# Optimization experiments

Measured on AMD Instinct MI355X. Metric: run time of the kernel, lower is better.

The kernel has to match this reference:

```python
import jax, jax.numpy as jnp
import numpy as np

N = 131072   # total nodes in batch
D = 128      # hidden dim (in_dim = out_dim = 128)
DX = 64      # raw node feature dim (x and rw_feature each)
NG = 1024    # number of graphs (global_add_pool segments)
E = 4194304  # edges per hop adjacency (avg degree 32)
H = 4        # num_hops + 1 MLP branches per layer


def setup_inputs() -> dict:
    key = jax.random.key(0)
    ks = jax.random.split(key, 16)
    s = 0.05
    return {
        "x": jax.random.normal(ks[0], (N, DX), jnp.float32),
        "rw_feature": jax.random.normal(ks[1], (N, DX), jnp.float32),
        "hop1_features": jax.random.normal(ks[2], (N, D), jnp.float32),
        "hop2_features": jax.random.normal(ks[3], (N, D), jnp.float32),
        "hop3_features": jax.random.normal(ks[4], (N, D), jnp.float32),
        "hop1_edges": jax.random.randint(ks[5], (2, E), 0, N, dtype=jnp.int32),
        "hop2_edges": jax.random.randint(ks[6], (2, E), 0, N, dtype=jnp.int32),
        "hop3_edges": jax.random.randint(ks[7], (2, E), 0, N, dtype=jnp.int32),
        "batch": jnp.sort(jax.random.randint(ks[8], (N,), 0, NG, dtype=jnp.int32)),
        "l1_w1": jax.random.normal(ks[9], (H, D, D), jnp.float32) * s,
        "l1_b1": jnp.zeros((H, D), jnp.float32),
        "l1_w2": jax.random.normal(ks[10], (H, D, D), jnp.float32) * s,
        "l1_b2": jnp.zeros((H, D), jnp.float32),
        "l2_w1": jax.random.normal(ks[11], (H, D, D), jnp.float32) * s,
        "l2_b1": jnp.zeros((H, D), jnp.float32),
        "l2_w2": jax.random.normal(ks[12], (H, D, D), jnp.float32) * s,
        "l2_b2": jnp.zeros((H, D), jnp.float32),
        "lin_w": jax.random.normal(ks[13], (2 * D, D), jnp.float32) * s,
        "lin_b": jnp.zeros((D,), jnp.float32),
    }


def _mhc_layer(hops, w1, b1, w2, b2):
    # hops: [H, N, D]; per-hop MLP (Linear -> ReLU -> Dropout(eval) -> Linear), summed over hops
    z = jax.nn.relu(jnp.einsum('hni,hio->hno', hops, w1) + b1[:, None, :])
    y = jnp.einsum('hno,hop->hnp', z, w2) + b2[:, None, :]
    return jnp.sum(y, axis=0)  # [N, D]


def _spmm(edges, x):
    # torch.sparse.mm(A, x) with A[r, c] = 1.0 per edge; duplicate edges accumulate (COO sum)
    return jax.ops.segment_sum(x[edges[1]], edges[0], num_segments=N)


def reference(x, rw_feature, hop1_features, hop2_features, hop3_features,
              hop1_edges, hop2_edges, hop3_edges, batch,
              l1_w1, l1_b1, l1_w2, l1_b2, l2_w1, l2_b1, l2_w2, l2_b2,
              lin_w, lin_b):
    f = jnp.concatenate([x, rw_feature], axis=1)  # [N, D]
    h1 = jnp.stack([f, hop1_features, hop2_features, hop3_features], axis=0)  # [H, N, D]
    x1 = _mhc_layer(h1, l1_w1, l1_b1, l1_w2, l1_b2)
    h2 = jnp.stack([x1,
                    _spmm(hop1_edges, x1),
                    _spmm(hop2_edges, x1),
                    _spmm(hop3_edges, x1)], axis=0)
    x2 = _mhc_layer(h2, l2_w1, l2_b1, l2_w2, l2_b2)
    out = jnp.concatenate([x1, x2], axis=1) @ lin_w + lin_b  # concat=True path
    return jax.ops.segment_sum(out, batch, num_segments=NG)  # global_add_pool -> [NG, D]
```

## Files before the change

kernel.cpp:

```cpp
#include <hip/hip_runtime.h>

#define N_NODES 131072
#define DIM     128
#define NGRAPH  1024
#define NEDGE   4194304

#define NW      512
#define WBINS   256
#define NSL     256
#define SLICE_E (NEDGE / NSL)
#define CAP     12288

typedef float floatx4 __attribute__((ext_vector_type(4)));
typedef float f32x4  __attribute__((ext_vector_type(4)));
typedef __bf16 bf16x8 __attribute__((ext_vector_type(8)));
typedef __bf16 bf16x4 __attribute__((ext_vector_type(4)));

__device__ __forceinline__ int lds_off(int row, int kb) {
    return row * 256 + (kb ^ ((row & 7) << 4));
}

__global__ __launch_bounds__(256)
void zero_kernel(floatx4* __restrict__ p, long n4) {
    long i = (long)blockIdx.x * blockDim.x + threadIdx.x;
    long stride = (long)gridDim.x * blockDim.x;
    floatx4 z = {0.f, 0.f, 0.f, 0.f};
    for (; i < n4; i += stride) p[i] = z;
}

__global__ __launch_bounds__(256)
void tr_kernel(const float* __restrict__ src, __bf16* __restrict__ dst, int nmat) {
    int idx = blockIdx.x * blockDim.x + threadIdx.x;
    int total = nmat * 16384;
    if (idx >= total) return;
    int m = idx >> 14;
    int col = (idx >> 7) & 127;
    int k = idx & 127;
    dst[idx] = (__bf16)src[m * 16384 + k * 128 + col];
}

__global__ __launch_bounds__(256)
void wincount_kernel(const int* __restrict__ e1, const int* __restrict__ e2,
                     const int* __restrict__ e3, int* __restrict__ gcount) {
    const int gb = blockIdx.x;
    const int sl = gb % NSL;
    const int hop = gb / NSL;
    const int* rows = hop == 0 ? e1 : hop == 1 ? e2 : e3;

    __shared__ int cnt[NW];
    for (int i = threadIdx.x; i < NW; i += 256) cnt[i] = 0;
    __syncthreads();

    const int4* src = (const int4*)rows + (size_t)sl * (SLICE_E / 4);
    for (int j = threadIdx.x; j < SLICE_E / 4; j += 256) {
        int4 v = src[j];
        atomicAdd(&cnt[v.x >> 8], 1); atomicAdd(&cnt[v.y >> 8], 1);
        atomicAdd(&cnt[v.z >> 8], 1); atomicAdd(&cnt[v.w >> 8], 1);
    }
    __syncthreads();

    int* dst = gcount + ((size_t)hop * NSL + sl) * NW;
    for (int i = threadIdx.x; i < NW; i += 256) dst[i] = cnt[i];
}

__global__ __launch_bounds__(256)
void basescan_kernel(const int* __restrict__ gcount, int* __restrict__ baseo,
                     int* __restrict__ wbase) {
    const int hop = blockIdx.x;
    const int t = threadIdx.x;
    __shared__ int wt[NW];
    __shared__ int part[256];

    for (int k = 0; k < 2; ++k) {
        int w = t * 2 + k;
        int s = 0;
        for (int sl = 0; sl < NSL; ++sl)
            s += gcount[((size_t)hop * NSL + sl) * NW + w];
        wt[w] = s;
    }
    __syncthreads();
    part[t] = wt[2 * t] + wt[2 * t + 1];
    __syncthreads();
    for (int d = 1; d < 256; d <<= 1) {
        int v = (t >= d) ? part[t - d] : 0;
        __syncthreads();
        part[t] += v;
        __syncthreads();
    }
    int run = (t == 0) ? 0 : part[t - 1];
    for (int k = 0; k < 2; ++k) {
        int w = 2 * t + k;
        wbase[hop * (NW + 1) + w] = run;
        int r2 = run;
        for (int sl = 0; sl < NSL; ++sl) {
            baseo[((size_t)hop * NW + w) * NSL + sl] = r2;
            r2 += gcount[((size_t)hop * NSL + sl) * NW + w];
        }
        run += wt[w];
    }
    if (t == 255) wbase[hop * (NW + 1) + NW] = NEDGE;
}

__global__ __launch_bounds__(256)
void bucket_kernel(const int* __restrict__ e1, const int* __restrict__ e2,
                   const int* __restrict__ e3, const int* __restrict__ baseo,
                   int* __restrict__ buf) {
    const int gb = blockIdx.x;
    const int sl = gb % NSL;
    const int hop = gb / NSL;
    const int* rows = hop == 0 ? e1 : hop == 1 ? e2 : e3;
    const int* cs = rows + NEDGE;

    __shared__ int cur[NW];
    for (int i = threadIdx.x; i < NW; i += 256)
        cur[i] = baseo[((size_t)hop * NW + i) * NSL + sl];
    __syncthreads();

    int* b = buf + (size_t)hop * NEDGE;
    const int4* r4 = (const int4*)rows + (size_t)sl * (SLICE_E / 4);
    const int4* c4 = (const int4*)cs + (size_t)sl * (SLICE_E / 4);
    for (int j = threadIdx.x; j < SLICE_E / 4; j += 256) {
        int4 r = r4[j];
        int4 c = c4[j];
        int p;
        p = atomicAdd(&cur[r.x >> 8], 1); b[p] = ((r.x & 255) << 17) | c.x;
        p = atomicAdd(&cur[r.y >> 8], 1); b[p] = ((r.y & 255) << 17) | c.y;
        p = atomicAdd(&cur[r.z >> 8], 1); b[p] = ((r.z & 255) << 17) | c.z;
        p = atomicAdd(&cur[r.w >> 8], 1); b[p] = ((r.w & 255) << 17) | c.w;
    }
}

__global__ __launch_bounds__(256)
void winbuild_kernel(const int* __restrict__ buf, const int* __restrict__ wbase,
                     int* __restrict__ offs3, int* __restrict__ cols) {
    const int gb = blockIdx.x;
    const int w = gb % NW;
    const int hop = gb / NW;
    const int b0 = wbase[hop * (NW + 1) + w];
    const int b1 = wbase[hop * (NW + 1) + w + 1];
    const int tot = b1 - b0;
    const int* src = buf + (size_t)hop * NEDGE + b0;
    int* col = cols + (size_t)hop * NEDGE;
    int* offs = offs3 + (size_t)hop * (N_NODES + 1);
    const int t = threadIdx.x;

    __shared__ int hist[WBINS];
    __shared__ int scanb[WBINS];
    __shared__ int image[CAP];

    hist[t] = 0;
    __syncthreads();
    for (int i = t; i < tot; i += 256) atomicAdd(&hist[src[i] >> 17], 1);
    __syncthreads();

    int v = hist[t];
    scanb[t] = v;
    __syncthreads();
    for (int d = 1; d < 256; d <<= 1) {
        int u = (t >= d) ? scanb[t - d] : 0;
        __syncthreads();
        scanb[t] += u;
        __syncthreads();
    }
    const int excl = scanb[t] - v;

    offs[w * WBINS + t] = b0 + excl;
    if (w == NW - 1 && t == 0) offs[N_NODES] = NEDGE;
    __syncthreads();

    if (tot <= CAP) {
        hist[t] = excl;
        __syncthreads();
        for (int i = t; i < tot; i += 256) {
            int e = src[i];
            int p = atomicAdd(&hist[e >> 17], 1);
            image[p] = e & 0x1FFFF;
        }
        __syncthreads();
        for (int i = t; i < tot; i += 256) col[b0 + i] = image[i];
    } else {
        hist[t] = b0 + excl;
        __syncthreads();
        for (int i = t; i < tot; i += 256) {
            int e = src[i];
            int p = atomicAdd(&hist[e >> 17], 1);
            col[p] = e & 0x1FFFF;
        }
    }
}

__global__ __launch_bounds__(256)
void csr_spmm_kernel(const int* __restrict__ offs, const int* __restrict__ col,
                     const __bf16* __restrict__ xin, __bf16* __restrict__ outb) {
    const int lane = threadIdx.x & 63;
    const int row = blockIdx.x * (blockDim.x >> 6) + (threadIdx.x >> 6);
    if (row >= N_NODES) return;
    const int beg = offs[row];
    const int end = offs[row + 1];

    float a0 = 0.f, a1 = 0.f, b0 = 0.f, b1 = 0.f;
    float c0f = 0.f, c1f = 0.f, d0 = 0.f, d1 = 0.f;
    for (int b = beg; b < end; b += 64) {
        const int n = min(64, end - b);
        int cidx = (b + lane < end) ? col[b + lane] : 0;
        int i = 0;
        for (; i + 4 <= n; i += 4) {
            int e0 = __shfl(cidx, i);
            int e1 = __shfl(cidx, i + 1);
            int e2 = __shfl(cidx, i + 2);
            int e3 = __shfl(cidx, i + 3);
            unsigned v0 = *(const unsigned*)(xin + (size_t)e0 * 128 + lane * 2);
            unsigned v1 = *(const unsigned*)(xin + (size_t)e1 * 128 + lane * 2);
            unsigned v2 = *(const unsigned*)(xin + (size_t)e2 * 128 + lane * 2);
            unsigned v3 = *(const unsigned*)(xin + (size_t)e3 * 128 + lane * 2);
            a0 += __uint_as_float(v0 << 16); a1 += __uint_as_float(v0 & 0xffff0000u);
            b0 += __uint_as_float(v1 << 16); b1 += __uint_as_float(v1 & 0xffff0000u);
            c0f += __uint_as_float(v2 << 16); c1f += __uint_as_float(v2 & 0xffff0000u);
            d0 += __uint_as_float(v3 << 16); d1 += __uint_as_float(v3 & 0xffff0000u);
        }
        for (; i < n; ++i) {
            int e = __shfl(cidx, i);
            unsigned v = *(const unsigned*)(xin + (size_t)e * 128 + lane * 2);
            a0 += __uint_as_float(v << 16); a1 += __uint_as_float(v & 0xffff0000u);
        }
    }
    float o0 = a0 + b0 + c0f + d0;
    float o1 = a1 + b1 + c1f + d1;
    union { unsigned u; __bf16 h[2]; } pk;
    pk.h[0] = (__bf16)o0; pk.h[1] = (__bf16)o1;
    *(unsigned*)(outb + (size_t)row * 128 + lane * 2) = pk.u;
}

__device__ __forceinline__ void stage_bf16_tile(char* dst, const __bf16* src, int tid) {
#pragma unroll
    for (int it = 0; it < 8; ++it) {
        int c = tid + it * 256;
        int r = c >> 4, o = c & 15;
        uint4 v = *(const uint4*)(src + (size_t)r * 128 + o * 8);
        *(uint4*)(dst + lds_off(r, o * 16)) = v;
    }
}

__device__ __forceinline__ void stage_f32_tile(char* dst, const float* src, int tid) {
#pragma unroll
    for (int it = 0; it < 16; ++it) {
        int c = tid + it * 256;
        int r = c >> 5, o = c & 31;
        floatx4 v = *(const floatx4*)(src + (size_t)r * 128 + o * 4);
        bf16x4 h;
        h[0] = (__bf16)v[0]; h[1] = (__bf16)v[1];
        h[2] = (__bf16)v[2]; h[3] = (__bf16)v[3];
        *(bf16x4*)(dst + lds_off(r, o * 8)) = h;
    }
}

__device__ __forceinline__ void mfma_relu_phase(char* az, const char* wb,
                                                const float* bias,
                                                int r0, int lrow, int grp) {
    bf16x8 am[2][4];
#pragma unroll
    for (int mt = 0; mt < 2; ++mt)
#pragma unroll
        for (int kk = 0; kk < 4; ++kk)
            am[mt][kk] = *(const bf16x8*)(az + lds_off(r0 + mt * 16 + lrow,
                                                       kk * 64 + grp * 16));
#pragma unroll
    for (int n = 0; n < 8; ++n) {
        f32x4 a0 = {0.f, 0.f, 0.f, 0.f};
        f32x4 a1 = {0.f, 0.f, 0.f, 0.f};
#pragma unroll
        for (int kk = 0; kk < 4; ++kk) {
            bf16x8 b = *(const bf16x8*)(wb + lds_off(n * 16 + lrow,
                                                     kk * 64 + grp * 16));
            a0 = __builtin_amdgcn_mfma_f32_16x16x32_bf16(am[0][kk], b, a0, 0, 0, 0);
            a1 = __builtin_amdgcn_mfma_f32_16x16x32_bf16(am[1][kk], b, a1, 0, 0, 0);
        }
        float bs = bias[n * 16 + lrow];
#pragma unroll
        for (int rg = 0; rg < 4; ++rg) {
            float v0 = fmaxf(a0[rg] + bs, 0.f);
            float v1 = fmaxf(a1[rg] + bs, 0.f);
            *(__bf16*)(az + lds_off(r0 + grp * 4 + rg, (n * 16 + lrow) * 2)) = (__bf16)v0;
            *(__bf16*)(az + lds_off(r0 + 16 + grp * 4 + rg, (n * 16 + lrow) * 2)) = (__bf16)v1;
        }
    }
}

__device__ __forceinline__ void mfma_phase(const char* az, const char* wb,
                                           int r0, int lrow, int grp,
                                           f32x4 (&acc)[2][8]) {
    bf16x8 am[2][4];
#pragma unroll
    for (int mt = 0; mt < 2; ++mt)
#pragma unroll
        for (int kk = 0; kk < 4; ++kk)
            am[mt][kk] = *(const bf16x8*)(az + lds_off(r0 + mt * 16 + lrow,
                                                       kk * 64 + grp * 16));
#pragma unroll
    for (int kk = 0; kk < 4; ++kk)
#pragma unroll
        for (int n = 0; n < 8; ++n) {
            bf16x8 b = *(const bf16x8*)(wb + lds_off(n * 16 + lrow,
                                                     kk * 64 + grp * 16));
#pragma unroll
            for (int mt = 0; mt < 2; ++mt)
                acc[mt][n] = __builtin_amdgcn_mfma_f32_16x16x32_bf16(
                    am[mt][kk], b, acc[mt][n], 0, 0, 0);
        }
}

__global__ __launch_bounds__(256, 2)
void layer1_kernel(const float* __restrict__ x, const float* __restrict__ rw,
                   const float* __restrict__ f1, const float* __restrict__ f2,
                   const float* __restrict__ f3,
                   const __bf16* __restrict__ wt1, const float* __restrict__ b1,
                   const __bf16* __restrict__ wt2, const float* __restrict__ b2,
                   __bf16* __restrict__ x1out)
{
    __shared__ uint4 lds_u4[4096];
    char* AZ = (char*)lds_u4;
    char* WB = (char*)lds_u4 + 32768;
    const int tid = threadIdx.x;
    const int lane = tid & 63;
    const int w = tid >> 6;
    const int r0 = w * 32;
    const int lrow = lane & 15;
    const int grp = lane >> 4;
    const int row0 = blockIdx.x * 128;

    f32x4 Y[2][8];
#pragma unroll
    for (int mt = 0; mt < 2; ++mt)
#pragma unroll
        for (int n = 0; n < 8; ++n) Y[mt][n] = {0.f, 0.f, 0.f, 0.f};

    for (int h = 0; h < 4; ++h) {
        __syncthreads();
        if (h == 0) {
#pragma unroll
            for (int it = 0; it < 16; ++it) {
                int c = tid + it * 256;
                int r = c >> 5, o = c & 31;
                const float* src = (o < 16)
                    ? (x  + (size_t)(row0 + r) * 64 + o * 4)
                    : (rw + (size_t)(row0 + r) * 64 + (o - 16) * 4);
                floatx4 v = *(const floatx4*)src;
                bf16x4 hh;
                hh[0] = (__bf16)v[0]; hh[1] = (__bf16)v[1];
                hh[2] = (__bf16)v[2]; hh[3] = (__bf16)v[3];
                *(bf16x4*)(AZ + lds_off(r, o * 8)) = hh;
            }
        } else {
            const float* feat = (h == 1) ? f1 : (h == 2) ? f2 : f3;
            stage_f32_tile(AZ, feat + (size_t)row0 * 128, tid);
        }
        stage_bf16_tile(WB, wt1 + (size_t)h * 16384, tid);
        __syncthreads();

        mfma_relu_phase(AZ, WB, b1 + h * 128, r0, lrow, grp);

        __syncthreads();
        stage_bf16_tile(WB, wt2 + (size_t)h * 16384, tid);
        __syncthreads();
        mfma_phase(AZ, WB, r0, lrow, grp, Y);
    }

#pragma unroll
    for (int n = 0; n < 8; ++n) {
        int cc = n * 16 + lrow;
        float bs = b2[cc] + b2[128 + cc] + b2[256 + cc] + b2[384 + cc];
#pragma unroll
        for (int mt = 0; mt < 2; ++mt)
#pragma unroll
            for (int rg = 0; rg < 4; ++rg) {
                int zr = r0 + mt * 16 + grp * 4 + rg;
                *(__bf16*)(AZ + lds_off(zr, cc * 2)) = (__bf16)(Y[mt][n][rg] + bs);
            }
    }
    __syncthreads();
#pragma unroll
    for (int it = 0; it < 8; ++it) {
        int f = tid + it * 256;
        int r = f >> 4, o = f & 15;
        uint4 v = *(const uint4*)(AZ + lds_off(r, o * 16));
        *(uint4*)(x1out + (size_t)(row0 + r) * 128 + o * 8) = v;
    }
}

__global__ __launch_bounds__(256, 2)
void layer2_kernel(const __bf16* __restrict__ x1b, const __bf16* __restrict__ s1,
                   const __bf16* __restrict__ s2, const __bf16* __restrict__ s3,
                   const __bf16* __restrict__ wt1, const float* __restrict__ b1,
                   const __bf16* __restrict__ wt2, const float* __restrict__ b2,
                   const __bf16* __restrict__ wtl, const float* __restrict__ linb,
                   const int* __restrict__ batch, float* __restrict__ dout)
{
    __shared__ uint4 lds_u4[4096];
    char* AZ = (char*)lds_u4;
    char* WB = (char*)lds_u4 + 32768;
    const int tid = threadIdx.x;
    const int lane = tid & 63;
    const int w = tid >> 6;
    const int r0 = w * 32;
    const int lrow = lane & 15;
    const int grp = lane >> 4;
    const int row0 = blockIdx.x * 128;

    f32x4 Y[2][8];
#pragma unroll
    for (int mt = 0; mt < 2; ++mt)
#pragma unroll
        for (int n = 0; n < 8; ++n) Y[mt][n] = {0.f, 0.f, 0.f, 0.f};

    for (int h = 0; h < 4; ++h) {
        const __bf16* feat = (h == 0) ? x1b : (h == 1) ? s1 : (h == 2) ? s2 : s3;
        __syncthreads();
        stage_bf16_tile(AZ, feat + (size_t)row0 * 128, tid);
        stage_bf16_tile(WB, wt1 + (size_t)h * 16384, tid);
        __syncthreads();

        mfma_relu_phase(AZ, WB, b1 + h * 128, r0, lrow, grp);

        __syncthreads();
        stage_bf16_tile(WB, wt2 + (size_t)h * 16384, tid);
        __syncthreads();
        mfma_phase(AZ, WB, r0, lrow, grp, Y);
    }

#pragma unroll
    for (int n = 0; n < 8; ++n) {
        int cc = n * 16 + lrow;
        float bs = b2[cc] + b2[128 + cc] + b2[256 + cc] + b2[384 + cc];
#pragma unroll
        for (int mt = 0; mt < 2; ++mt)
#pragma unroll
            for (int rg = 0; rg < 4; ++rg) {
                float v = Y[mt][n][rg] + bs;
                int zr = r0 + mt * 16 + grp * 4 + rg;
                *(__bf16*)(AZ + lds_off(zr, (n * 16 + lrow) * 2)) = (__bf16)v;
            }
    }
    __syncthreads();
    stage_bf16_tile(WB, wtl + 16384, tid);
    __syncthreads();

    f32x4 o[2][8];
#pragma unroll
    for (int mt = 0; mt < 2; ++mt)
#pragma unroll
        for (int n = 0; n < 8; ++n) o[mt][n] = {0.f, 0.f, 0.f, 0.f};
    mfma_phase(AZ, WB, r0, lrow, grp, o);

    __syncthreads();
    stage_bf16_tile(AZ, x1b + (size_t)row0 * 128, tid);
    stage_bf16_tile(WB, wtl, tid);
    __syncthreads();
    mfma_phase(AZ, WB, r0, lrow, grp, o);

    __syncthreads();
    float* tile32 = (float*)lds_u4;
#pragma unroll
    for (int n = 0; n < 8; ++n) {
        int cc = n * 16 + lrow;
        float lb = linb[cc];
#pragma unroll
        for (int mt = 0; mt < 2; ++mt)
#pragma unroll
            for (int rg = 0; rg < 4; ++rg) {
                int rl = r0 + mt * 16 + grp * 4 + rg;
                tile32[rl * 128 + cc] = o[mt][n][rg] + lb;
            }
    }
    __syncthreads();

    if (tid < 128) {
        const int d = tid;
        float acc = 0.f;
        int cur = batch[row0];
        for (int r = 0; r < 128; ++r) {
            int b = batch[row0 + r];
            if (b != cur) {
                atomicAdd(dout + (size_t)cur * 128 + d, acc);
                acc = 0.f;
                cur = b;
            }
            acc += tile32[r * 128 + d];
        }
        atomicAdd(dout + (size_t)cur * 128 + d, acc);
    }
}

extern "C" void kernel_launch(void* const* d_in, const int* in_sizes, int n_in,
                              void* d_out, int out_size, void* d_ws, size_t ws_size,
                              hipStream_t stream) {
    (void)in_sizes; (void)n_in; (void)out_size; (void)ws_size;

    const float* x    = (const float*)d_in[0];
    const float* rw   = (const float*)d_in[1];
    const float* f1   = (const float*)d_in[2];
    const float* f2   = (const float*)d_in[3];
    const float* f3   = (const float*)d_in[4];
    const int*   e1   = (const int*)d_in[5];
    const int*   e2   = (const int*)d_in[6];
    const int*   e3   = (const int*)d_in[7];
    const int*   batch= (const int*)d_in[8];
    const float* l1w1 = (const float*)d_in[9];
    const float* l1b1 = (const float*)d_in[10];
    const float* l1w2 = (const float*)d_in[11];
    const float* l1b2 = (const float*)d_in[12];
    const float* l2w1 = (const float*)d_in[13];
    const float* l2b1 = (const float*)d_in[14];
    const float* l2w2 = (const float*)d_in[15];
    const float* l2b2 = (const float*)d_in[16];
    const float* linw = (const float*)d_in[17];
    const float* linb = (const float*)d_in[18];

    float* out = (float*)d_out;

    __bf16* x1b = (__bf16*)d_ws;
    __bf16* s1b = x1b + (size_t)N_NODES * 128;
    __bf16* s2b = s1b + (size_t)N_NODES * 128;
    __bf16* s3b = s2b + (size_t)N_NODES * 128;
    __bf16* wt  = s3b + (size_t)N_NODES * 128;
    __bf16* wt_l1w1 = wt;
    __bf16* wt_l1w2 = wt + 4 * 16384;
    __bf16* wt_l2w1 = wt + 8 * 16384;
    __bf16* wt_l2w2 = wt + 12 * 16384;
    __bf16* wt_lin  = wt + 16 * 16384;
    int* ibase  = (int*)(wt + 18 * 16384);
    int* offs3  = ibase;
    int* gcount = offs3 + (size_t)3 * (N_NODES + 1);
    int* baseo  = gcount + (size_t)3 * NSL * NW;
    int* wbase  = baseo + (size_t)3 * NW * NSL;
    int* buf    = wbase + (size_t)3 * (NW + 1);
    int* cols   = buf + (size_t)3 * NEDGE;

    tr_kernel<<<256, 256, 0, stream>>>(l1w1, wt_l1w1, 4);
    tr_kernel<<<256, 256, 0, stream>>>(l1w2, wt_l1w2, 4);
    tr_kernel<<<256, 256, 0, stream>>>(l2w1, wt_l2w1, 4);
    tr_kernel<<<256, 256, 0, stream>>>(l2w2, wt_l2w2, 4);
    tr_kernel<<<128, 256, 0, stream>>>(linw, wt_lin, 2);

    zero_kernel<<<64, 256, 0, stream>>>((floatx4*)out, (long)NGRAPH * 32);

    layer1_kernel<<<N_NODES / 128, 256, 0, stream>>>(
        x, rw, f1, f2, f3, wt_l1w1, l1b1, wt_l1w2, l1b2, x1b);

    wincount_kernel<<<3 * NSL, 256, 0, stream>>>(e1, e2, e3, gcount);
    basescan_kernel<<<3, 256, 0, stream>>>(gcount, baseo, wbase);
    bucket_kernel<<<3 * NSL, 256, 0, stream>>>(e1, e2, e3, baseo, buf);
    winbuild_kernel<<<3 * NW, 256, 0, stream>>>(buf, wbase, offs3, cols);

    __bf16* ss[3] = {s1b, s2b, s3b};
    for (int hop = 0; hop < 3; ++hop) {
        csr_spmm_kernel<<<N_NODES / 4, 256, 0, stream>>>(
            offs3 + (size_t)hop * (N_NODES + 1), cols + (size_t)hop * NEDGE,
            x1b, ss[hop]);
    }

    layer2_kernel<<<N_NODES / 128, 256, 0, stream>>>(
        x1b, s1b, s2b, s3b, wt_l2w1, l2b1, wt_l2w2, l2b2, wt_lin, linb, batch, out);
}
```

Measured before the change: 978.0 us.

## Pre-convert layer1 inputs to bf16 and stage tiles via direct global-to-LDS loads

```diff
diff --git a/kernel.cpp b/kernel.cpp
--- a/kernel.cpp
+++ b/kernel.cpp
@@ -20,12 +20,61 @@
     return row * 256 + (kb ^ ((row & 7) << 4));
 }
 
+#define GLOAD16(gp, lp) __builtin_amdgcn_global_load_lds( \
+    (const __attribute__((address_space(1))) void*)(gp),  \
+    (__attribute__((address_space(3))) void*)(lp), 16, 0, 0)
+
+__device__ __forceinline__ void stage_async(char* dstbase, const char* src,
+                                            int w, int lane) {
+#pragma unroll
+    for (int it = 0; it < 8; ++it) {
+        int chunk = it * 4 + w;
+        int p = chunk * 1024 + lane * 16;
+        int r = p >> 8;
+        int o = p & 255;
+        const char* g = src + r * 256 + (o ^ ((r & 7) << 4));
+        GLOAD16(g, dstbase + chunk * 1024);
+    }
+}
+
 __global__ __launch_bounds__(256)
 void zero_kernel(floatx4* __restrict__ p, long n4) {
     long i = (long)blockIdx.x * blockDim.x + threadIdx.x;
     long stride = (long)gridDim.x * blockDim.x;
     floatx4 z = {0.f, 0.f, 0.f, 0.f};
     for (; i < n4; i += stride) p[i] = z;
+}
+
+__global__ __launch_bounds__(256)
+void cvt_kernel(const float* __restrict__ src, __bf16* __restrict__ dst) {
+    int i = blockIdx.x * 256 + threadIdx.x;
+    const int stride = gridDim.x * 256;
+    const int total = N_NODES * 32;
+    for (; i < total; i += stride) {
+        floatx4 v = ((const floatx4*)src)[i];
+        bf16x4 h;
+        h[0] = (__bf16)v[0]; h[1] = (__bf16)v[1];
+        h[2] = (__bf16)v[2]; h[3] = (__bf16)v[3];
+        ((bf16x4*)dst)[i] = h;
+    }
+}
+
+__global__ __launch_bounds__(256)
+void cvt_cat_kernel(const float* __restrict__ x, const float* __restrict__ rw,
+                    __bf16* __restrict__ dst) {
+    int i = blockIdx.x * 256 + threadIdx.x;
+    const int stride = gridDim.x * 256;
+    const int total = N_NODES * 32;
+    for (; i < total; i += stride) {
+        int rowg = i >> 5, g = i & 31;
+        const float* s = (g < 16) ? x  + (size_t)rowg * 64 + g * 4
+                                  : rw + (size_t)rowg * 64 + (g - 16) * 4;
+        floatx4 v = *(const floatx4*)s;
+        bf16x4 h;
+        h[0] = (__bf16)v[0]; h[1] = (__bf16)v[1];
+        h[2] = (__bf16)v[2]; h[3] = (__bf16)v[3];
+        *(bf16x4*)(dst + (size_t)rowg * 128 + g * 4) = h;
+    }
 }
 
 __global__ __launch_bounds__(256)
@@ -231,29 +280,6 @@
     *(unsigned*)(outb + (size_t)row * 128 + lane * 2) = pk.u;
 }
 
-__device__ __forceinline__ void stage_bf16_tile(char* dst, const __bf16* src, int tid) {
-#pragma unroll
-    for (int it = 0; it < 8; ++it) {
-        int c = tid + it * 256;
-        int r = c >> 4, o = c & 15;
-        uint4 v = *(const uint4*)(src + (size_t)r * 128 + o * 8);
-        *(uint4*)(dst + lds_off(r, o * 16)) = v;
-    }
-}
-
-__device__ __forceinline__ void stage_f32_tile(char* dst, const float* src, int tid) {
-#pragma unroll
-    for (int it = 0; it < 16; ++it) {
-        int c = tid + it * 256;
-        int r = c >> 5, o = c & 31;
-        floatx4 v = *(const floatx4*)(src + (size_t)r * 128 + o * 4);
-        bf16x4 h;
-        h[0] = (__bf16)v[0]; h[1] = (__bf16)v[1];
-        h[2] = (__bf16)v[2]; h[3] = (__bf16)v[3];
-        *(bf16x4*)(dst + lds_off(r, o * 8)) = h;
-    }
-}
-
 __device__ __forceinline__ void mfma_relu_phase(char* az, const char* wb,
                                                 const float* bias,
                                                 int r0, int lrow, int grp) {
@@ -310,9 +336,8 @@
 }
 
 __global__ __launch_bounds__(256, 2)
-void layer1_kernel(const float* __restrict__ x, const float* __restrict__ rw,
-                   const float* __restrict__ f1, const float* __restrict__ f2,
-                   const float* __restrict__ f3,
+void layer1_kernel(const __bf16* __restrict__ xr, const __bf16* __restrict__ f1,
+                   const __bf16* __restrict__ f2, const __bf16* __restrict__ f3,
                    const __bf16* __restrict__ wt1, const float* __restrict__ b1,
                    const __bf16* __restrict__ wt2, const float* __restrict__ b2,
                    __bf16* __restrict__ x1out)
@@ -335,32 +360,16 @@
         for (int n = 0; n < 8; ++n) Y[mt][n] = {0.f, 0.f, 0.f, 0.f};
 
     for (int h = 0; h < 4; ++h) {
-        __syncthreads();
-        if (h == 0) {
-#pragma unroll
-            for (int it = 0; it < 16; ++it) {
-                int c = tid + it * 256;
-                int r = c >> 5, o = c & 31;
-                const float* src = (o < 16)
-                    ? (x  + (size_t)(row0 + r) * 64 + o * 4)
-                    : (rw + (size_t)(row0 + r) * 64 + (o - 16) * 4);
-                floatx4 v = *(const floatx4*)src;
-                bf16x4 hh;
-                hh[0] = (__bf16)v[0]; hh[1] = (__bf16)v[1];
-                hh[2] = (__bf16)v[2]; hh[3] = (__bf16)v[3];
-                *(bf16x4*)(AZ + lds_off(r, o * 8)) = hh;
-            }
-        } else {
-            const float* feat = (h == 1) ? f1 : (h == 2) ? f2 : f3;
-            stage_f32_tile(AZ, feat + (size_t)row0 * 128, tid);
-        }
-        stage_bf16_tile(WB, wt1 + (size_t)h * 16384, tid);
+        const __bf16* feat = (h == 0) ? xr : (h == 1) ? f1 : (h == 2) ? f2 : f3;
+        __syncthreads();
+        stage_async(AZ, (const char*)(feat + (size_t)row0 * 128), w, lane);
+        stage_async(WB, (const char*)(wt1 + (size_t)h * 16384), w, lane);
         __syncthreads();
 
         mfma_relu_phase(AZ, WB, b1 + h * 128, r0, lrow, grp);
 
         __syncthreads();
-        stage_bf16_tile(WB, wt2 + (size_t)h * 16384, tid);
+        stage_async(WB, (const char*)(wt2 + (size_t)h * 16384), w, lane);
         __syncthreads();
         mfma_phase(AZ, WB, r0, lrow, grp, Y);
     }
@@ -415,14 +424,14 @@
     for (int h = 0; h < 4; ++h) {
         const __bf16* feat = (h == 0) ? x1b : (h == 1) ? s1 : (h == 2) ? s2 : s3;
         __syncthreads();
-        stage_bf16_tile(AZ, feat + (size_t)row0 * 128, tid);
-        stage_bf16_tile(WB, wt1 + (size_t)h * 16384, tid);
+        stage_async(AZ, (const char*)(feat + (size_t)row0 * 128), w, lane);
+        stage_async(WB, (const char*)(wt1 + (size_t)h * 16384), w, lane);
         __syncthreads();
 
         mfma_relu_phase(AZ, WB, b1 + h * 128, r0, lrow, grp);
 
         __syncthreads();
-        stage_bf16_tile(WB, wt2 + (size_t)h * 16384, tid);
+        stage_async(WB, (const char*)(wt2 + (size_t)h * 16384), w, lane);
         __syncthreads();
         mfma_phase(AZ, WB, r0, lrow, grp, Y);
     }
@@ -441,7 +450,7 @@
             }
     }
     __syncthreads();
-    stage_bf16_tile(WB, wtl + 16384, tid);
+    stage_async(WB, (const char*)(wtl + 16384), w, lane);
     __syncthreads();
 
     f32x4 o[2][8];
@@ -452,8 +461,8 @@
     mfma_phase(AZ, WB, r0, lrow, grp, o);
 
     __syncthreads();
-    stage_bf16_tile(AZ, x1b + (size_t)row0 * 128, tid);
-    stage_bf16_tile(WB, wtl, tid);
+    stage_async(AZ, (const char*)(x1b + (size_t)row0 * 128), w, lane);
+    stage_async(WB, (const char*)wtl, w, lane);
     __syncthreads();
     mfma_phase(AZ, WB, r0, lrow, grp, o);
 
@@ -534,6 +543,7 @@
     int* wbase  = baseo + (size_t)3 * NW * NSL;
     int* buf    = wbase + (size_t)3 * (NW + 1);
     int* cols   = buf + (size_t)3 * NEDGE;
+    __bf16* xrb = (__bf16*)buf;
 
     tr_kernel<<<256, 256, 0, stream>>>(l1w1, wt_l1w1, 4);
     tr_kernel<<<256, 256, 0, stream>>>(l1w2, wt_l1w2, 4);
@@ -541,10 +551,15 @@
     tr_kernel<<<256, 256, 0, stream>>>(l2w2, wt_l2w2, 4);
     tr_kernel<<<128, 256, 0, stream>>>(linw, wt_lin, 2);
 
+    cvt_cat_kernel<<<4096, 256, 0, stream>>>(x, rw, xrb);
+    cvt_kernel<<<4096, 256, 0, stream>>>(f1, s1b);
+    cvt_kernel<<<4096, 256, 0, stream>>>(f2, s2b);
+    cvt_kernel<<<4096, 256, 0, stream>>>(f3, s3b);
+
     zero_kernel<<<64, 256, 0, stream>>>((floatx4*)out, (long)NGRAPH * 32);
 
     layer1_kernel<<<N_NODES / 128, 256, 0, stream>>>(
-        x, rw, f1, f2, f3, wt_l1w1, l1b1, wt_l1w2, l1b2, x1b);
+        xrb, s1b, s2b, s3b, wt_l1w1, l1b1, wt_l1w2, l1b2, x1b);
 
     wincount_kernel<<<3 * NSL, 256, 0, stream>>>(e1, e2, e3, gcount);
     basescan_kernel<<<3, 256, 0, stream>>>(gcount, baseo, wbase);
```

After: 958.1 us. 2.0% less time.
